# Kernel optimization log

Hardware: AMD Instinct MI355X
Metric: run time of the kernel (lower is better)

The kernel has to match this reference:

```python
import jax, jax.numpy as jnp
import numpy as np
from jax import lax

DN = ('NCDHW', 'OIDHW', 'NCDHW')  # dimension numbers matching torch Conv3d (cross-correlation)


def setup_inputs() -> dict:
    key = jax.random.key(0)
    k0, k1, k2, k3 = jax.random.split(key, 4)
    B, P, C = 32, 2048, 512
    x = jax.random.normal(k0, (B, P, C), dtype=jnp.float32)
    w1 = jax.random.normal(k1, (1, 1, 1, 1, 1), dtype=jnp.float32)
    w2 = jax.random.normal(k2, (1, 1, 2, 2, 2), dtype=jnp.float32)
    w3 = jax.random.normal(k3, (1, 1, 3, 3, 3), dtype=jnp.float32)
    return {"x": x, "w1": w1, "w2": w2, "w3": w3}


def reference(x, w1, w2, w3):
    B, P, C = x.shape
    t = P // 16
    # [B,P,C] -> [B,C,t,4,4]
    xv = jnp.transpose(x, (0, 2, 1)).reshape(B, C, t, 4, 4)
    # x_shift: [B,t,C,4,4] -> [B*t, C, 4, 4]
    x_shift = jnp.transpose(xv, (0, 2, 1, 3, 4)).reshape(B * t, C, 4, 4)
    # channel mean -> [B,1,t,4,4]
    xm = jnp.mean(xv, axis=1, keepdims=True)
    # ST_1: 1x1x1 conv, no pad
    p1 = lax.conv_general_dilated(xm, w1, (1, 1, 1), 'VALID', dimension_numbers=DN)
    # ST_2: pad (left=1 on t,h,w), then 2x2x2 valid conv -> same shape
    xp = jnp.pad(xm, ((0, 0), (0, 0), (1, 0), (1, 0), (1, 0)))
    p2 = lax.conv_general_dilated(xp, w2, (1, 1, 1), 'VALID', dimension_numbers=DN)
    # ST_3: 3x3x3 conv with padding 1 -> same shape
    p3 = lax.conv_general_dilated(xm, w3, (1, 1, 1), [(1, 1), (1, 1), (1, 1)], dimension_numbers=DN)
    g = p1 + p2 + p3  # [B,1,t,4,4]
    # transpose(2,1) -> [B,t,1,4,4] -> [B*t,1,4,4]
    g = jnp.transpose(g, (0, 2, 1, 3, 4)).reshape(B * t, 1, 4, 4)
    out = x_shift * jax.nn.sigmoid(g)  # broadcast over C
    # back to [B,P,C]
    out = out.reshape(B, t, C, 4, 4)
    out = jnp.transpose(out, (0, 2, 1, 3, 4)).reshape(B, C, P)
    return jnp.transpose(out, (0, 2, 1))
```

## Files before the change

kernel.cpp:

```cpp
#include <hip/hip_runtime.h>
#include <math.h>

#define BB 32
#define PP 2048
#define CC 512
#define TT 128
#define NROWS (BB*PP)
#define NTILES (BB*TT)

__global__ __launch_bounds__(256) void mean_kernel(
        const float* __restrict__ x, float* __restrict__ mean) {
    __shared__ float spart[4][8];
    int bid  = blockIdx.x;
    int tid  = threadIdx.x;
    int wave = tid >> 6;
    int lane = tid & 63;

    const float4* xt = (const float4*)x + (size_t)bid * 2048;
    float p[8];
    #pragma unroll
    for (int j = 0; j < 8; ++j) {
        float4 v = xt[tid + 256 * j];
        p[j] = (v.x + v.y) + (v.z + v.w);
    }
    #pragma unroll
    for (int j = 0; j < 8; ++j) {
        float s = p[j];
        #pragma unroll
        for (int off = 32; off > 0; off >>= 1)
            s += __shfl_down(s, off, 64);
        if (lane == 0) spart[wave][j] = s;
    }
    __syncthreads();
    if (tid < 16) {
        int jj = tid >> 1;
        float s = (tid & 1) ? (spart[2][jj] + spart[3][jj])
                            : (spart[0][jj] + spart[1][jj]);
        mean[bid * 16 + tid] = s * (1.0f / 512.0f);
    }
}

__global__ __launch_bounds__(256) void gate_scale_kernel(
        const float* __restrict__ x, const float* __restrict__ mean,
        const float* __restrict__ w1, const float* __restrict__ w2,
        const float* __restrict__ w3, float* __restrict__ out) {
    __shared__ float sm[3][16];
    __shared__ float sgate[16];
    int bid = blockIdx.x;
    int b = bid >> 7;
    int t = bid & 127;
    int tid = threadIdx.x;

    if (tid < 48) {
        int plane = tid >> 4;
        int r     = tid & 15;
        int tv    = t + plane - 1;
        sm[plane][r] = (tv >= 0 && tv < TT)
                         ? mean[(b * TT + tv) * 16 + r] : 0.0f;
    }
    __syncthreads();

    if (tid < 16) {
        int h  = tid >> 2;
        int w_ = tid & 3;
        float g = 0.0f;
        #pragma unroll
        for (int i = 0; i < 3; ++i) {
            #pragma unroll
            for (int j = 0; j < 3; ++j) {
                int hh = h + j - 1;
                if (hh < 0 || hh > 3) continue;
                #pragma unroll
                for (int k = 0; k < 3; ++k) {
                    int ww = w_ + k - 1;
                    if (ww < 0 || ww > 3) continue;
                    float wt = w3[i * 9 + j * 3 + k];
                    if (i < 2 && j < 2 && k < 2) wt += w2[i * 4 + j * 2 + k];
                    if (i == 1 && j == 1 && k == 1) wt += w1[0];
                    g += wt * sm[i][hh * 4 + ww];
                }
            }
        }
        sgate[tid] = 1.0f / (1.0f + __expf(-g));
    }
    __syncthreads();

    const float4* xt = (const float4*)x + (size_t)bid * 2048;
    float4*       ot = (float4*)out     + (size_t)bid * 2048;
    #pragma unroll
    for (int j = 0; j < 8; ++j) {
        int idx = tid + 256 * j;
        float s = sgate[idx >> 7];
        float4 v = xt[idx];
        v.x *= s; v.y *= s; v.z *= s; v.w *= s;
        ot[idx] = v;
    }
}

extern "C" void kernel_launch(void* const* d_in, const int* in_sizes, int n_in,
                              void* d_out, int out_size, void* d_ws, size_t ws_size,
                              hipStream_t stream) {
    const float* x  = (const float*)d_in[0];
    const float* w1 = (const float*)d_in[1];
    const float* w2 = (const float*)d_in[2];
    const float* w3 = (const float*)d_in[3];
    float* out  = (float*)d_out;
    float* mean = (float*)d_ws;

    mean_kernel<<<NTILES, 256, 0, stream>>>(x, mean);
    gate_scale_kernel<<<NTILES, 256, 0, stream>>>(x, mean, w1, w2, w3, out);
}
```

Measured before the change: 254.7 us.

## Fuse mean and gate-scale kernels with register-held tiles and halo recompute

Replaces the two-kernel pipeline (channel mean to workspace, then gate and scale) with one kernel where each block processes two consecutive t-slices, holding their data in registers for both the mean and the scaled write. Neighbouring slice means needed by the 3x3x3 conv are recomputed from halo reads of adjacent slices rather than from a workspace. A block-index swizzle groups neighbouring chunks to improve cache reuse of halo reads. This removes the second full read of x and one launch, but adds redundant halo traffic and register pressure.

```diff
diff --git a/kernel.cpp b/kernel.cpp
--- a/kernel.cpp
+++ b/kernel.cpp
@@ -5,64 +5,81 @@
 #define PP 2048
 #define CC 512
 #define TT 128
-#define NROWS (BB*PP)
-#define NTILES (BB*TT)
+#define NCHUNK 64
+#define NBLK (BB*NCHUNK)
 
-__global__ __launch_bounds__(256) void mean_kernel(
-        const float* __restrict__ x, float* __restrict__ mean) {
-    __shared__ float spart[4][8];
-    int bid  = blockIdx.x;
-    int tid  = threadIdx.x;
-    int wave = tid >> 6;
-    int lane = tid & 63;
-
-    const float4* xt = (const float4*)x + (size_t)bid * 2048;
-    float p[8];
-    #pragma unroll
-    for (int j = 0; j < 8; ++j) {
-        float4 v = xt[tid + 256 * j];
-        p[j] = (v.x + v.y) + (v.z + v.w);
-    }
-    #pragma unroll
-    for (int j = 0; j < 8; ++j) {
-        float s = p[j];
-        #pragma unroll
-        for (int off = 32; off > 0; off >>= 1)
-            s += __shfl_down(s, off, 64);
-        if (lane == 0) spart[wave][j] = s;
-    }
-    __syncthreads();
-    if (tid < 16) {
-        int jj = tid >> 1;
-        float s = (tid & 1) ? (spart[2][jj] + spart[3][jj])
-                            : (spart[0][jj] + spart[1][jj]);
-        mean[bid * 16 + tid] = s * (1.0f / 512.0f);
-    }
-}
-
-__global__ __launch_bounds__(256) void gate_scale_kernel(
-        const float* __restrict__ x, const float* __restrict__ mean,
+__global__ __launch_bounds__(256, 4) void fused2_kernel(
+        const float* __restrict__ x,
         const float* __restrict__ w1, const float* __restrict__ w2,
         const float* __restrict__ w3, float* __restrict__ out) {
-    __shared__ float sm[3][16];
-    __shared__ float sgate[16];
+    __shared__ float sm[4][16];
+    __shared__ float sg[32];
+
     int bid = blockIdx.x;
-    int b = bid >> 7;
-    int t = bid & 127;
+    int wg  = ((bid & 7) << 8) | (bid >> 3);
+    int b  = wg >> 6;
+    int c  = wg & 63;
+    int t0 = c << 1;
+
     int tid = threadIdx.x;
+    int row = tid >> 4;
+    int seg = tid & 15;
 
-    if (tid < 48) {
-        int plane = tid >> 4;
-        int r     = tid & 15;
-        int tv    = t + plane - 1;
-        sm[plane][r] = (tv >= 0 && tv < TT)
-                         ? mean[(b * TT + tv) * 16 + r] : 0.0f;
+    const float4* xb = (const float4*)x + (size_t)b * (PP * CC / 4);
+    const float4* xp0 = xb + (size_t)t0 * 2048;
+    const float4* xp1 = xp0 + 2048;
+
+    float4 v0[8], v1[8];
+    #pragma unroll
+    for (int k = 0; k < 8; ++k) v0[k] = xp0[row * 128 + seg + 16 * k];
+    #pragma unroll
+    for (int k = 0; k < 8; ++k) v1[k] = xp1[row * 128 + seg + 16 * k];
+
+    int hr     = tid >> 3;
+    int hu     = tid & 7;
+    int hplane = hr >> 4;
+    int hrow   = hr & 15;
+    int ht     = hplane ? (t0 + 2) : (t0 - 1);
+    bool hv    = (ht >= 0) && (ht < TT);
+    float ha = 0.0f, hb2 = 0.0f;
+    if (hv) {
+        const float4* hp = xb + (size_t)ht * 2048 + hrow * 128;
+        #pragma unroll
+        for (int k = 0; k < 8; ++k) {
+            float4 u = hp[hu + 8 * (2 * k)];
+            float4 w = hp[hu + 8 * (2 * k + 1)];
+            ha  += (u.x + u.y) + (u.z + u.w);
+            hb2 += (w.x + w.y) + (w.z + w.w);
+        }
     }
+    float hs = ha + hb2;
+    hs += __shfl_xor(hs, 1, 64);
+    hs += __shfl_xor(hs, 2, 64);
+    hs += __shfl_xor(hs, 4, 64);
+
+    float s0 = 0.0f, s1 = 0.0f;
+    #pragma unroll
+    for (int k = 0; k < 8; ++k) s0 += (v0[k].x + v0[k].y) + (v0[k].z + v0[k].w);
+    #pragma unroll
+    for (int k = 0; k < 8; ++k) s1 += (v1[k].x + v1[k].y) + (v1[k].z + v1[k].w);
+    #pragma unroll
+    for (int m = 1; m <= 8; m <<= 1) {
+        s0 += __shfl_xor(s0, m, 64);
+        s1 += __shfl_xor(s1, m, 64);
+    }
+
+    if (seg == 0) {
+        sm[1][row] = s0 * (1.0f / 512.0f);
+        sm[2][row] = s1 * (1.0f / 512.0f);
+    }
+    if (hu == 0) sm[hplane ? 3 : 0][hrow] = hv ? hs * (1.0f / 512.0f) : 0.0f;
     __syncthreads();
 
-    if (tid < 16) {
-        int h  = tid >> 2;
-        int w_ = tid & 3;
+    if (tid < 32) {
+        int q  = tid >> 4;
+        int r  = tid & 15;
+        int h  = r >> 2;
+        int w_ = r & 3;
         float g = 0.0f;
         #pragma unroll
         for (int i = 0; i < 3; ++i) {
@@ -77,23 +94,28 @@
                     float wt = w3[i * 9 + j * 3 + k];
                     if (i < 2 && j < 2 && k < 2) wt += w2[i * 4 + j * 2 + k];
                     if (i == 1 && j == 1 && k == 1) wt += w1[0];
-                    g += wt * sm[i][hh * 4 + ww];
+                    g += wt * sm[q + i][hh * 4 + ww];
                 }
             }
         }
-        sgate[tid] = 1.0f / (1.0f + __expf(-g));
+        sg[tid] = 1.0f / (1.0f + __expf(-g));
     }
     __syncthreads();
 
-    const float4* xt = (const float4*)x + (size_t)bid * 2048;
-    float4*       ot = (float4*)out     + (size_t)bid * 2048;
+    float g0 = sg[row];
+    float g1 = sg[16 + row];
+    float4* ob = (float4*)out + (size_t)b * (PP * CC / 4) + (size_t)t0 * 2048;
     #pragma unroll
-    for (int j = 0; j < 8; ++j) {
-        int idx = tid + 256 * j;
-        float s = sgate[idx >> 7];
-        float4 v = xt[idx];
-        v.x *= s; v.y *= s; v.z *= s; v.w *= s;
-        ot[idx] = v;
+    for (int k = 0; k < 8; ++k) {
+        float4 o = v0[k];
+        o.x *= g0; o.y *= g0; o.z *= g0; o.w *= g0;
+        ob[row * 128 + seg + 16 * k] = o;
+    }
+    #pragma unroll
+    for (int k = 0; k < 8; ++k) {
+        float4 o = v1[k];
+        o.x *= g1; o.y *= g1; o.z *= g1; o.w *= g1;
+        ob[2048 + row * 128 + seg + 16 * k] = o;
     }
 }
 
@@ -104,9 +126,7 @@
     const float* w1 = (const float*)d_in[1];
     const float* w2 = (const float*)d_in[2];
     const float* w3 = (const float*)d_in[3];
-    float* out  = (float*)d_out;
-    float* mean = (float*)d_ws;
+    float* out = (float*)d_out;
 
-    mean_kernel<<<NTILES, 256, 0, stream>>>(x, mean);
-    gate_scale_kernel<<<NTILES, 256, 0, stream>>>(x, mean, w1, w2, w3, out);
+    fused2_kernel<<<NBLK, 256, 0, stream>>>(x, w1, w2, w3, out);
 }
```

Result: faster. 245.2 us (-3.7%).

## Fuse mean and gate-scale into one cooperative kernel with grid sync

Applied to the files above, without the earlier changes.

Replaces the two-kernel mean/gate pipeline with a single cooperative kernel. Each block computes channel means for four planes, a grid-wide sync follows, and then the block computes gates and scales the same four planes. The second read of x is intended to hit in cache (the 128MB input may partly fit in MI355X last-level cache) and one launch is removed. It adds a grid sync and requires all 1024 blocks of 512 threads to be co-resident, with a fallback to the old two-kernel path if the cooperative launch fails.

```diff
diff --git a/kernel.cpp b/kernel.cpp
--- a/kernel.cpp
+++ b/kernel.cpp
@@ -1,68 +1,71 @@
 #include <hip/hip_runtime.h>
+#include <hip/hip_cooperative_groups.h>
 #include <math.h>
+
+namespace cg = cooperative_groups;
 
 #define BB 32
 #define PP 2048
 #define CC 512
 #define TT 128
-#define NROWS (BB*PP)
-#define NTILES (BB*TT)
+#define PLANES (BB*TT)
+#define PPB 4
+#define NBLK (PLANES/PPB)
+#define THR 512
 
-__global__ __launch_bounds__(256) void mean_kernel(
-        const float* __restrict__ x, float* __restrict__ mean) {
-    __shared__ float spart[4][8];
-    int bid  = blockIdx.x;
-    int tid  = threadIdx.x;
-    int wave = tid >> 6;
-    int lane = tid & 63;
+__global__ __launch_bounds__(THR, 8) void coop_kernel(
+        const float* __restrict__ x,
+        const float* __restrict__ w1, const float* __restrict__ w2,
+        const float* __restrict__ w3, float* __restrict__ out,
+        float* __restrict__ wsmean) {
+    __shared__ float sm[6][16];
+    __shared__ float sgate[64];
 
-    const float4* xt = (const float4*)x + (size_t)bid * 2048;
-    float p[8];
+    int bid = blockIdx.x;
+    int wg  = ((bid & 7) << 7) | (bid >> 3);
+    int b   = wg >> 5;
+    int t0  = (wg & 31) << 2;
+    int plane0 = b * TT + t0;
+
+    int tid = threadIdx.x;
+    int row = tid >> 3;
+    int seg = tid & 7;
+
+    const float4* xr = (const float4*)x + (size_t)plane0 * 2048 + row * 128;
+
+    float a0 = 0.f, a1 = 0.f, a2 = 0.f, a3 = 0.f;
     #pragma unroll
-    for (int j = 0; j < 8; ++j) {
-        float4 v = xt[tid + 256 * j];
-        p[j] = (v.x + v.y) + (v.z + v.w);
+    for (int k = 0; k < 4; ++k) {
+        float4 u = xr[seg + 8 * (4 * k + 0)];
+        float4 v = xr[seg + 8 * (4 * k + 1)];
+        float4 p = xr[seg + 8 * (4 * k + 2)];
+        float4 q = xr[seg + 8 * (4 * k + 3)];
+        a0 += (u.x + u.y) + (u.z + u.w);
+        a1 += (v.x + v.y) + (v.z + v.w);
+        a2 += (p.x + p.y) + (p.z + p.w);
+        a3 += (q.x + q.y) + (q.z + q.w);
     }
-    #pragma unroll
-    for (int j = 0; j < 8; ++j) {
-        float s = p[j];
-        #pragma unroll
-        for (int off = 32; off > 0; off >>= 1)
-            s += __shfl_down(s, off, 64);
-        if (lane == 0) spart[wave][j] = s;
+    float s = (a0 + a1) + (a2 + a3);
+    s += __shfl_xor(s, 1, 64);
+    s += __shfl_xor(s, 2, 64);
+    s += __shfl_xor(s, 4, 64);
+    if (seg == 0) wsmean[plane0 * 16 + row] = s * (1.0f / 512.0f);
+
+    __threadfence();
+    cg::this_grid().sync();
+
+    if (tid < 96) {
+        int q = tid >> 4;
+        int r = tid & 15;
+        int tq = t0 + q - 1;
+        sm[q][r] = (tq >= 0 && tq < TT) ? wsmean[(b * TT + tq) * 16 + r] : 0.0f;
     }
     __syncthreads();
-    if (tid < 16) {
-        int jj = tid >> 1;
-        float s = (tid & 1) ? (spart[2][jj] + spart[3][jj])
-                            : (spart[0][jj] + spart[1][jj]);
-        mean[bid * 16 + tid] = s * (1.0f / 512.0f);
-    }
-}
-
-__global__ __launch_bounds__(256) void gate_scale_kernel(
-        const float* __restrict__ x, const float* __restrict__ mean,
-        const float* __restrict__ w1, const float* __restrict__ w2,
-        const float* __restrict__ w3, float* __restrict__ out) {
-    __shared__ float sm[3][16];
-    __shared__ float sgate[16];
-    int bid = blockIdx.x;
-    int b = bid >> 7;
-    int t = bid & 127;
-    int tid = threadIdx.x;
-
-    if (tid < 48) {
-        int plane = tid >> 4;
-        int r     = tid & 15;
-        int tv    = t + plane - 1;
-        sm[plane][r] = (tv >= 0 && tv < TT)
-                         ? mean[(b * TT + tv) * 16 + r] : 0.0f;
-    }
-    __syncthreads();
-
-    if (tid < 16) {
-        int h  = tid >> 2;
-        int w_ = tid & 3;
+    if (tid < 64) {
+        int q  = tid >> 4;
+        int r  = tid & 15;
+        int h  = r >> 2;
+        int w_ = r & 3;
         float g = 0.0f;
         #pragma unroll
         for (int i = 0; i < 3; ++i) {
@@ -77,7 +80,7 @@
                     float wt = w3[i * 9 + j * 3 + k];
                     if (i < 2 && j < 2 && k < 2) wt += w2[i * 4 + j * 2 + k];
                     if (i == 1 && j == 1 && k == 1) wt += w1[0];
-                    g += wt * sm[i][hh * 4 + ww];
+                    g += wt * sm[q + i][hh * 4 + ww];
                 }
             }
         }
@@ -85,6 +88,79 @@
     }
     __syncthreads();
 
+    float g = sgate[row];
+    float4* op = (float4*)out + (size_t)plane0 * 2048 + row * 128;
+    #pragma unroll
+    for (int k = 0; k < 16; ++k) {
+        float4 v = xr[seg + 8 * k];
+        v.x *= g; v.y *= g; v.z *= g; v.w *= g;
+        op[seg + 8 * k] = v;
+    }
+}
+
+__global__ __launch_bounds__(256) void mean_fb(
+        const float* __restrict__ x, float* __restrict__ mean) {
+    __shared__ float spart[4][8];
+    int bid = blockIdx.x, tid = threadIdx.x;
+    int wave = tid >> 6, lane = tid & 63;
+    const float4* xt = (const float4*)x + (size_t)bid * 2048;
+    float p[8];
+    #pragma unroll
+    for (int j = 0; j < 8; ++j) {
+        float4 v = xt[tid + 256 * j];
+        p[j] = (v.x + v.y) + (v.z + v.w);
+    }
+    #pragma unroll
+    for (int j = 0; j < 8; ++j) {
+        float s = p[j];
+        #pragma unroll
+        for (int off = 32; off > 0; off >>= 1) s += __shfl_down(s, off, 64);
+        if (lane == 0) spart[wave][j] = s;
+    }
+    __syncthreads();
+    if (tid < 16) {
+        int jj = tid >> 1;
+        float s = (tid & 1) ? (spart[2][jj] + spart[3][jj])
+                            : (spart[0][jj] + spart[1][jj]);
+        mean[bid * 16 + tid] = s * (1.0f / 512.0f);
+    }
+}
+
+__global__ __launch_bounds__(256) void gate_scale_fb(
+        const float* __restrict__ x, const float* __restrict__ mean,
+        const float* __restrict__ w1, const float* __restrict__ w2,
+        const float* __restrict__ w3, float* __restrict__ out) {
+    __shared__ float sm[3][16];
+    __shared__ float sgate[16];
+    int bid = blockIdx.x;
+    int b = bid >> 7, t = bid & 127, tid = threadIdx.x;
+    if (tid < 48) {
+        int plane = tid >> 4, r = tid & 15, tv = t + plane - 1;
+        sm[plane][r] = (tv >= 0 && tv < TT) ? mean[(b * TT + tv) * 16 + r] : 0.0f;
+    }
+    __syncthreads();
+    if (tid < 16) {
+        int h = tid >> 2, w_ = tid & 3;
+        float g = 0.0f;
+        #pragma unroll
+        for (int i = 0; i < 3; ++i)
+            #pragma unroll
+            for (int j = 0; j < 3; ++j) {
+                int hh = h + j - 1;
+                if (hh < 0 || hh > 3) continue;
+                #pragma unroll
+                for (int k = 0; k < 3; ++k) {
+                    int ww = w_ + k - 1;
+                    if (ww < 0 || ww > 3) continue;
+                    float wt = w3[i * 9 + j * 3 + k];
+                    if (i < 2 && j < 2 && k < 2) wt += w2[i * 4 + j * 2 + k];
+                    if (i == 1 && j == 1 && k == 1) wt += w1[0];
+                    g += wt * sm[i][hh * 4 + ww];
+                }
+            }
+        sgate[tid] = 1.0f / (1.0f + __expf(-g));
+    }
+    __syncthreads();
     const float4* xt = (const float4*)x + (size_t)bid * 2048;
     float4*       ot = (float4*)out     + (size_t)bid * 2048;
     #pragma unroll
@@ -107,6 +183,12 @@
     float* out  = (float*)d_out;
     float* mean = (float*)d_ws;
 
-    mean_kernel<<<NTILES, 256, 0, stream>>>(x, mean);
-    gate_scale_kernel<<<NTILES, 256, 0, stream>>>(x, mean, w1, w2, w3, out);
+    void* args[] = {(void*)&x, (void*)&w1, (void*)&w2, (void*)&w3,
+                    (void*)&out, (void*)&mean};
+    hipError_t err = hipLaunchCooperativeKernel(
+        (const void*)coop_kernel, dim3(NBLK), dim3(THR), args, 0, stream);
+    if (err != hipSuccess) {
+        mean_fb<<<PLANES, 256, 0, stream>>>(x, mean);
+        gate_scale_fb<<<PLANES, 256, 0, stream>>>(x, mean, w1, w2, w3, out);
+    }
 }
```

Result: slower. 688.6 us (+170.4%).
